# Kernel optimization log

Measured on AMD Instinct MI355X. Metric: run time of the kernel, lower is better.

The kernel has to match this reference:

```python
import jax, jax.numpy as jnp
import numpy as np
from math import sqrt


def _build_transitions(dim):
    # Upper-triangular (i<=j) pairs in the same row-major order as the torch loop.
    iu0, iu1 = np.triu_indices(dim)
    n_mono = len(iu0)
    idx = np.arange(n_mono)
    M = np.zeros((dim, dim), dtype=np.int32)
    M[iu0, iu1] = idx
    M[iu1, iu0] = idx
    coef_trans = np.full((n_mono, 1), sqrt(2.0), dtype=np.float32)
    coef_trans[idx[iu0 == iu1]] = 1.0  # diagonal coefficients stay scale 1
    return iu0, iu1, M.reshape(-1), coef_trans


def setup_inputs() -> dict:
    key = jax.random.key(0)
    k1, k2, k3, k4 = jax.random.split(key, 4)
    dim, n_quadrics, B = 512, 64, 2048
    n_mono = dim * (dim - 1) // 2 + dim  # 131328
    points = jax.random.normal(k1, (B, dim), dtype=jnp.float32)
    # orthogonal-ish init is only an init detail; random normal keeps math identical
    q_coefs = jax.random.normal(k2, (n_mono, n_quadrics), dtype=jnp.float32) / np.sqrt(n_mono)
    l_coefs = 2.0 * jax.random.uniform(k3, (dim, n_quadrics), dtype=jnp.float32) - 1.0
    free_coefs = 2.0 * jax.random.uniform(k4, (1, n_quadrics), dtype=jnp.float32) - 1.0
    return {"points": points, "q_coefs": q_coefs, "l_coefs": l_coefs, "free_coefs": free_coefs}


def reference(points, q_coefs, l_coefs, free_coefs):
    B, dim = points.shape
    nq = q_coefs.shape[1]
    iu0, iu1, inds_trans, coef_trans_np = _build_transitions(dim)
    coef_trans = jnp.asarray(coef_trans_np)

    # quadratic monomials: q[b, k] = p[b, i_k] * p[b, j_k]  (upper-tri order)
    q = points[:, iu0] * points[:, iu1]  # (B, n_mono)

    coefs = q_coefs * coef_trans  # (n_mono, nq) real coefficients

    # values of quadrics at points
    values = jnp.abs(q @ coefs + points @ l_coefs + free_coefs)  # (B, nq)

    # symmetric full matrices gathered from flat coefficient vector
    m_full = coefs[inds_trans].reshape(dim, dim, nq)  # (dim, dim, nq)
    dm = (jnp.eye(dim, dtype=points.dtype) + 1.0)[:, :, None]  # 2 on diag, ... wait: eye+ones -> 2 diag, 1 off
    m_scaled = m_full * dm

    # gradients: grad[b, k, e] = sum_d p[b, d] * m_scaled[d, e, k] + l_coefs[e, k]
    q_grad = jnp.einsum("bd,dek->bke", points, m_scaled) + l_coefs.T[None, :, :]  # (B, nq, dim)
    grad = jnp.sum(q_grad * q_grad, axis=2)  # (B, nq)

    norm = jnp.linalg.norm(q_coefs, axis=0)  # (nq,)
    scores = (jnp.sqrt(grad / 4.0 + values * norm) - jnp.sqrt(grad) / 2.0) / norm
    return scores
```

## Files before the change

kernel.cpp:

```cpp
#include <hip/hip_runtime.h>

#define DIM 512
#define NQ 64
#define BATCH 2048

typedef __bf16  bf16x8  __attribute__((ext_vector_type(8)));
typedef float   floatx4 __attribute__((ext_vector_type(4)));

static __device__ inline unsigned short f2bf(float f) {
    unsigned int u = __float_as_uint(f);
    return (unsigned short)((u + 0x7fffu + ((u >> 16) & 1u)) >> 16);
}
static __device__ inline float bf2f(unsigned short h) {
    return __uint_as_float((unsigned int)h << 16);
}
static __device__ inline unsigned int pack2(float a, float b) {
    return (unsigned)f2bf(a) | ((unsigned)f2bf(b) << 16);
}

__global__ __launch_bounds__(512, 3)
void hsq_expand_kernel(const float* __restrict__ qc,
                       const float* __restrict__ pts,
                       unsigned short* __restrict__ W,
                       unsigned short* __restrict__ Pb,
                       float* __restrict__ npart) {
    const int e = blockIdx.x;

    if (blockIdx.y == 4) {
        const int i4 = e * 512 + threadIdx.x;
        const float4 v = *(const float4*)(pts + (size_t)i4 * 4);
        uint2 wv;
        wv.x = pack2(v.x, v.y); wv.y = pack2(v.z, v.w);
        *(uint2*)(Pb + (size_t)i4 * 4) = wv;
        return;
    }

    const int dblk = blockIdx.y;
    const int pb   = dblk * 512 + e;
    const int wid  = threadIdx.x >> 6;
    const int k    = threadIdx.x & 63;
    const int d0   = dblk * 128 + wid * 16;

    __shared__ unsigned short tv[64 * 136];
    __shared__ float part[8][64];

    float v[16];
#pragma unroll
    for (int s = 0; s < 16; ++s) {
        const int d = d0 + s;
        const int i = d < e ? d : e;
        const int j = d < e ? e : d;
        const int idx = i * DIM - ((i * (i - 1)) >> 1) + (j - i);
        v[s] = qc[(size_t)idx * NQ + k];
    }

    float nacc = 0.0f;
#pragma unroll
    for (int s = 0; s < 16; ++s)
        if (d0 + s >= e) nacc += v[s] * v[s];

#pragma unroll
    for (int t = 0; t < 2; ++t) {
        float sc[8];
#pragma unroll
        for (int q = 0; q < 8; ++q) {
            const int d = d0 + t * 8 + q;
            sc[q] = v[t * 8 + q] * ((d == e) ? 2.0f : 1.41421356237309515f);
        }
        uint4 w;
        w.x = pack2(sc[0], sc[1]); w.y = pack2(sc[2], sc[3]);
        w.z = pack2(sc[4], sc[5]); w.w = pack2(sc[6], sc[7]);
        *(uint4*)&tv[k * 136 + wid * 16 + t * 8] = w;
    }
    part[wid][k] = nacc;
    __syncthreads();

#pragma unroll
    for (int r = 0; r < 2; ++r) {
        const int kk = r * 32 + (threadIdx.x >> 4);
        const int u  = threadIdx.x & 15;
        const uint4 w = *(const uint4*)&tv[kk * 136 + u * 8];
        *(uint4*)(W + ((size_t)(kk * DIM + e)) * DIM + dblk * 128 + u * 8) = w;
    }
    if (threadIdx.x < 64) {
        npart[(size_t)k * 2048 + pb] =
            part[0][k] + part[1][k] + part[2][k] + part[3][k] +
            part[4][k] + part[5][k] + part[6][k] + part[7][k];
    }
}

__global__ __launch_bounds__(512, 2)
void hsq_gemm_kernel(const unsigned short* __restrict__ Pb,
                     const unsigned short* __restrict__ W,
                     const float* __restrict__ l_coefs,
                     float2* __restrict__ part) {
    extern __shared__ unsigned short smem[];

    const int bid = blockIdx.x;
    const int wg  = (bid & 7) * 128 + (bid >> 3);
    const int k   = wg >> 4;
    const int rem = wg & 15;
    const int et  = rem >> 3;
    const int mt  = rem & 7;
    const int m0  = mt * 256;

    const int tid  = threadIdx.x;
    const int lane = tid & 63;
    const int w    = tid >> 6;
    const int wm   = w >> 2;
    const int wn   = w & 3;
    const int c    = lane & 15;
    const int quad = lane >> 4;

    const unsigned short* Wk = W + ((size_t)k * DIM + (size_t)et * 256) * DIM;

    const int scolb = ((tid & 7) * 16) ^ (((tid >> 3) & 7) << 4);
    const unsigned short* pAs = Pb + (size_t)(m0 + (tid >> 3)) * DIM + (scolb >> 1);
    const unsigned short* pBs = Wk + (size_t)(tid >> 3) * DIM + (scolb >> 1);

    const int xorv  = (c & 7) << 4;
    const int koff0 = ((0 * 64 + quad * 16) ^ xorv) >> 1;
    const int koff1 = ((1 * 64 + quad * 16) ^ xorv) >> 1;
    const int awoff = wm * 8192 + c * 64;
    const int bwoff = (wn >> 1) * 8192 + (wn & 1) * 4096 + c * 64;

#define STAGE_HALF(LDSELEM, GSRC) do {                                         \
    _Pragma("unroll")                                                          \
    for (int cc_ = 0; cc_ < 2; ++cc_) {                                        \
        __builtin_amdgcn_global_load_lds(                                      \
            (const __attribute__((address_space(1))) unsigned int*)            \
                ((GSRC) + (size_t)(cc_ * 64) * DIM),                           \
            (__attribute__((address_space(3))) unsigned int*)                  \
                (smem + (LDSELEM) + cc_ * 4096 + tid * 8),                     \
            16, 0, 0);                                                         \
    }                                                                          \
} while (0)

#define LOADB(BBASE) do {                                                      \
    _Pragma("unroll")                                                          \
    for (int ni_ = 0; ni_ < 4; ++ni_) {                                        \
        bfr[ni_][0] = *(const bf16x8*)(smem + (BBASE) + bwoff + ni_ * 1024 + koff0); \
        bfr[ni_][1] = *(const bf16x8*)(smem + (BBASE) + bwoff + ni_ * 1024 + koff1); \
    }                                                                          \
} while (0)

#define PHASE(ABASE, MI0, PRE_B, STAGE_AND_WAIT) do {                          \
    bf16x8 a00 = *(const bf16x8*)(smem + (ABASE) + awoff + (MI0) * 1024 + koff0);     \
    bf16x8 a01 = *(const bf16x8*)(smem + (ABASE) + awoff + (MI0) * 1024 + koff1);     \
    bf16x8 a10 = *(const bf16x8*)(smem + (ABASE) + awoff + ((MI0) + 1) * 1024 + koff0); \
    bf16x8 a11 = *(const bf16x8*)(smem + (ABASE) + awoff + ((MI0) + 1) * 1024 + koff1); \
    PRE_B;                                                                     \
    STAGE_AND_WAIT;                                                            \
    asm volatile("" ::: "memory");                                             \
    __builtin_amdgcn_s_barrier();                                              \
    asm volatile("" ::: "memory");                                             \
    __builtin_amdgcn_s_setprio(1);                                             \
    _Pragma("unroll")                                                          \
    for (int ni_ = 0; ni_ < 4; ++ni_) {                                        \
        acc[(MI0)][ni_]     = __builtin_amdgcn_mfma_f32_16x16x32_bf16(a00, bfr[ni_][0], acc[(MI0)][ni_], 0, 0, 0);     \
        acc[(MI0)][ni_]     = __builtin_amdgcn_mfma_f32_16x16x32_bf16(a01, bfr[ni_][1], acc[(MI0)][ni_], 0, 0, 0);     \
        acc[(MI0) + 1][ni_] = __builtin_amdgcn_mfma_f32_16x16x32_bf16(a10, bfr[ni_][0], acc[(MI0) + 1][ni_], 0, 0, 0); \
        acc[(MI0) + 1][ni_] = __builtin_amdgcn_mfma_f32_16x16x32_bf16(a11, bfr[ni_][1], acc[(MI0) + 1][ni_], 0, 0, 0); \
    }                                                                          \
    __builtin_amdgcn_s_setprio(0);                                             \
    asm volatile("" ::: "memory");                                             \
    __builtin_amdgcn_s_barrier();                                              \
    asm volatile("" ::: "memory");                                             \
} while (0)

    floatx4 acc[8][4];
#pragma unroll
    for (int mi = 0; mi < 8; ++mi)
#pragma unroll
        for (int ni = 0; ni < 4; ++ni)
            acc[mi][ni] = (floatx4){0.f, 0.f, 0.f, 0.f};

    bf16x8 bfr[4][2];

    STAGE_HALF(0,             pAs);
    STAGE_HALF(8192,          pAs + 128 * DIM);
    STAGE_HALF(16384,         pBs);
    STAGE_HALF(16384 + 8192,  pBs + 128 * DIM);
    STAGE_HALF(49152,         pBs + 64);
    STAGE_HALF(49152 + 8192,  pBs + 128 * DIM + 64);
    asm volatile("s_waitcnt vmcnt(4)" ::: "memory");
    __builtin_amdgcn_s_barrier();
    asm volatile("" ::: "memory");

    for (int it = 0; it < 4; ++it) {
        const unsigned short* pA1 = pAs + (size_t)(2 * it + 1) * 64;
        const unsigned short* pB2 = pBs + (size_t)(2 * it + 2) * 64;
        const unsigned short* pA2 = pAs + (size_t)(2 * it + 2) * 64;
        const unsigned short* pB3 = pBs + (size_t)(2 * it + 3) * 64;

        PHASE(0, 0, LOADB(16384), { STAGE_HALF(32768, pA1); });
        PHASE(0, 2, ((void)0),    { STAGE_HALF(32768 + 8192, pA1 + 128 * DIM); });
        PHASE(0, 4, ((void)0),    { if (it < 3) STAGE_HALF(16384, pB2); });
        PHASE(0, 6, ((void)0), {
            if (it < 3) {
                STAGE_HALF(16384 + 8192, pB2 + 128 * DIM);
                asm volatile("s_waitcnt vmcnt(4)" ::: "memory");
            } else {
                asm volatile("s_waitcnt vmcnt(0)" ::: "memory");
            }
        });
        PHASE(32768, 0, LOADB(49152), { if (it < 3) STAGE_HALF(0, pA2); });
        PHASE(32768, 2, ((void)0),    { if (it < 3) STAGE_HALF(8192, pA2 + 128 * DIM); });
        PHASE(32768, 4, ((void)0),    { if (it < 3) STAGE_HALF(49152, pB3); });
        PHASE(32768, 6, ((void)0), {
            if (it < 3) {
                STAGE_HALF(49152 + 8192, pB3 + 128 * DIM);
                asm volatile("s_waitcnt vmcnt(4)" ::: "memory");
            }
        });
    }
#undef PHASE
#undef LOADB
#undef STAGE_HALF

    __syncthreads();

    float lcv[4];
#pragma unroll
    for (int ni = 0; ni < 4; ++ni)
        lcv[ni] = l_coefs[(et * 256 + wn * 64 + ni * 16 + c) * NQ + k];

    const unsigned short* Pe = Pb + (size_t)(m0 + wm * 128) * DIM + et * 256 + wn * 64 + c;
    float* red = (float*)smem;

#pragma unroll
    for (int mi = 0; mi < 8; ++mi)
#pragma unroll
        for (int r = 0; r < 4; ++r) {
            const unsigned short* Prow = Pe + (size_t)(mi * 16 + quad * 4 + r) * DIM;
            float pv = 0.f, pg = 0.f;
#pragma unroll
            for (int ni = 0; ni < 4; ++ni) {
                const float g = acc[mi][ni][r];
                const float l = lcv[ni];
                pv += bf2f(Prow[ni * 16]) * (0.5f * g + l);
                const float gq = g + l;
                pg += gq * gq;
            }
#pragma unroll
            for (int off = 1; off < 16; off <<= 1) {
                pv += __shfl_xor(pv, off);
                pg += __shfl_xor(pg, off);
            }
            if (c == 0) {
                const int row16 = mi * 16 + quad * 4 + r;
                red[(w * 128 + row16) * 2 + 0] = pv;
                red[(w * 128 + row16) * 2 + 1] = pg;
            }
        }
    __syncthreads();

    if (tid < 256) {
        const int row16 = tid & 127;
        const int wmf   = tid >> 7;
        float pv = 0.f, pg = 0.f;
#pragma unroll
        for (int wnf = 0; wnf < 4; ++wnf) {
            const int wi = wmf * 4 + wnf;
            pv += red[(wi * 128 + row16) * 2 + 0];
            pg += red[(wi * 128 + row16) * 2 + 1];
        }
        part[((size_t)(et * NQ + k)) * BATCH + m0 + wmf * 128 + row16] =
            make_float2(pv, pg);
    }
}

__global__ void hsq_final_kernel(const float2* __restrict__ part,
                                 const float* __restrict__ npart,
                                 const float* __restrict__ free_coefs,
                                 float* __restrict__ out) {
    const int k = blockIdx.x;
    const int t = threadIdx.x;
    __shared__ float ws[4];

    const float4* src = (const float4*)(npart + (size_t)k * 2048);
    const float4 a = src[t * 2], b = src[t * 2 + 1];
    float s = a.x + a.y + a.z + a.w + b.x + b.y + b.z + b.w;
#pragma unroll
    for (int off = 1; off < 64; off <<= 1) s += __shfl_xor(s, off);
    if ((t & 63) == 0) ws[t >> 6] = s;
    __syncthreads();
    const float nrm = sqrtf(ws[0] + ws[1] + ws[2] + ws[3]);
    const float fc  = free_coefs[k];

#pragma unroll
    for (int i = 0; i < 8; ++i) {
        const int bidx = i * 256 + t;
        float pv = 0.f, pg = 0.f;
#pragma unroll
        for (int eb = 0; eb < 2; ++eb) {
            const float2 p = part[((size_t)(eb * NQ + k)) * BATCH + bidx];
            pv += p.x; pg += p.y;
        }
        const float vals = fabsf(pv + fc);
        out[(size_t)bidx * NQ + k] = (sqrtf(0.25f * pg + vals * nrm) - 0.5f * sqrtf(pg)) / nrm;
    }
}

extern "C" void kernel_launch(void* const* d_in, const int* in_sizes, int n_in,
                              void* d_out, int out_size, void* d_ws, size_t ws_size,
                              hipStream_t stream) {
    const float* points     = (const float*)d_in[0];
    const float* q_coefs    = (const float*)d_in[1];
    const float* l_coefs    = (const float*)d_in[2];
    const float* free_coefs = (const float*)d_in[3];
    float* out = (float*)d_out;

    char* ws = (char*)d_ws;
    unsigned short* W  = (unsigned short*)ws;
    unsigned short* Pb = (unsigned short*)(ws + 33554432);
    float2*         part  = (float2*)(ws + 35651584);
    float*          npart = (float*)(ws + 37748736);

    static bool attr_done = false;
    if (!attr_done) {
        (void)hipFuncSetAttribute((const void*)hsq_gemm_kernel,
                                  hipFuncAttributeMaxDynamicSharedMemorySize,
                                  131072);
        attr_done = true;
    }

    hsq_expand_kernel<<<dim3(512, 5), 512, 0, stream>>>(q_coefs, points, W, Pb, npart);
    hsq_gemm_kernel<<<dim3(1024), dim3(512), 131072, stream>>>(Pb, W, l_coefs, part);
    hsq_final_kernel<<<dim3(NQ), 256, 0, stream>>>(part, npart, free_coefs, out);
}
```

Before: 191.6 us.

## Shrink GEMM tile to 256x128 with triple-buffered K=32 pipeline

The gradient GEMM now splits each quadric's output dimension into four 128-wide tiles instead of two 256-wide tiles. This doubles the grid to 2048 blocks and halves the per-wave accumulator set to 4x4 MFMA tiles. K is staged in 32-element chunks through a three-slot LDS ring using direct global-to-LDS loads, with a new swizzle. LDS per block drops from 128 KB to about 76 KB, and launch bounds are raised to target more resident waves. In exchange, the tiles are less arithmetically intense, more barriers are issued per K, and the partial-sum buffer and final reduction grow to four e-blocks.

```diff
diff --git a/kernel.cpp b/kernel.cpp
--- a/kernel.cpp
+++ b/kernel.cpp
@@ -89,7 +89,7 @@
     }
 }
 
-__global__ __launch_bounds__(512, 2)
+__global__ __launch_bounds__(512, 4)
 void hsq_gemm_kernel(const unsigned short* __restrict__ Pb,
                      const unsigned short* __restrict__ W,
                      const float* __restrict__ l_coefs,
@@ -97,9 +97,9 @@
     extern __shared__ unsigned short smem[];
 
     const int bid = blockIdx.x;
-    const int wg  = (bid & 7) * 128 + (bid >> 3);
-    const int k   = wg >> 4;
-    const int rem = wg & 15;
+    const int wg  = (bid & 7) * 256 + (bid >> 3);
+    const int k   = wg >> 5;
+    const int rem = wg & 31;
     const int et  = rem >> 3;
     const int mt  = rem & 7;
     const int m0  = mt * 256;
@@ -107,129 +107,128 @@
     const int tid  = threadIdx.x;
     const int lane = tid & 63;
     const int w    = tid >> 6;
-    const int wm   = w >> 2;
-    const int wn   = w & 3;
+    const int wm   = w >> 1;
+    const int wn   = w & 1;
     const int c    = lane & 15;
     const int quad = lane >> 4;
 
-    const unsigned short* Wk = W + ((size_t)k * DIM + (size_t)et * 256) * DIM;
-
-    const int scolb = ((tid & 7) * 16) ^ (((tid >> 3) & 7) << 4);
-    const unsigned short* pAs = Pb + (size_t)(m0 + (tid >> 3)) * DIM + (scolb >> 1);
-    const unsigned short* pBs = Wk + (size_t)(tid >> 3) * DIM + (scolb >> 1);
-
-    const int xorv  = (c & 7) << 4;
-    const int koff0 = ((0 * 64 + quad * 16) ^ xorv) >> 1;
-    const int koff1 = ((1 * 64 + quad * 16) ^ xorv) >> 1;
-    const int awoff = wm * 8192 + c * 64;
-    const int bwoff = (wn >> 1) * 8192 + (wn & 1) * 4096 + c * 64;
-
-#define STAGE_HALF(LDSELEM, GSRC) do {                                         \
+    const unsigned short* aptr0;
+    const unsigned short* aptr1;
+    const unsigned short* bptr;
+    {
+        int slot = tid;
+        int p = slot >> 3;
+        int x = ((slot & 7) ^ (p & 7)) << 4;
+        aptr0 = Pb + (size_t)(m0 + (p << 1) + (x >> 6)) * DIM + ((x & 63) >> 1);
+        slot = 512 + tid;
+        p = slot >> 3;
+        x = ((slot & 7) ^ (p & 7)) << 4;
+        aptr1 = Pb + (size_t)(m0 + (p << 1) + (x >> 6)) * DIM + ((x & 63) >> 1);
+        slot = tid;
+        p = slot >> 3;
+        x = ((slot & 7) ^ (p & 7)) << 4;
+        bptr = W + (size_t)k * DIM * DIM
+                 + (size_t)(et * 128 + (p << 1) + (x >> 6)) * DIM + ((x & 63) >> 1);
+    }
+
+    int aoff[4], boff[4];
+#pragma unroll
+    for (int mi = 0; mi < 4; ++mi) {
+        const int row  = wm * 64 + mi * 16 + c;
+        const int line = row >> 1;
+        const int inb  = (((row & 1) << 6) | (quad << 4)) ^ ((line & 7) << 4);
+        aoff[mi] = line * 64 + (inb >> 1);
+    }
+#pragma unroll
+    for (int ni = 0; ni < 4; ++ni) {
+        const int row  = wn * 64 + ni * 16 + c;
+        const int line = row >> 1;
+        const int inb  = (((row & 1) << 6) | (quad << 4)) ^ ((line & 7) << 4);
+        boff[ni] = line * 64 + (inb >> 1);
+    }
+
+#define STAGE3(SB, T) do {                                                     \
+    __builtin_amdgcn_global_load_lds(                                          \
+        (const __attribute__((address_space(1))) unsigned int*)(aptr0 + (T) * 32), \
+        (__attribute__((address_space(3))) unsigned int*)(smem + (SB) * 12288 + tid * 8), \
+        16, 0, 0);                                                             \
+    __builtin_amdgcn_global_load_lds(                                          \
+        (const __attribute__((address_space(1))) unsigned int*)(aptr1 + (T) * 32), \
+        (__attribute__((address_space(3))) unsigned int*)(smem + (SB) * 12288 + 4096 + tid * 8), \
+        16, 0, 0);                                                             \
+    __builtin_amdgcn_global_load_lds(                                          \
+        (const __attribute__((address_space(1))) unsigned int*)(bptr + (T) * 32), \
+        (__attribute__((address_space(3))) unsigned int*)(smem + (SB) * 12288 + 8192 + tid * 8), \
+        16, 0, 0);                                                             \
+} while (0)
+
+#define KITER(TB, STAGE_STMT, WAIT_STMT) do {                                  \
+    STAGE_STMT;                                                                \
+    bf16x8 afr[4], bfr[4];                                                     \
     _Pragma("unroll")                                                          \
-    for (int cc_ = 0; cc_ < 2; ++cc_) {                                        \
-        __builtin_amdgcn_global_load_lds(                                      \
-            (const __attribute__((address_space(1))) unsigned int*)            \
-                ((GSRC) + (size_t)(cc_ * 64) * DIM),                           \
-            (__attribute__((address_space(3))) unsigned int*)                  \
-                (smem + (LDSELEM) + cc_ * 4096 + tid * 8),                     \
-            16, 0, 0);                                                         \
-    }                                                                          \
-} while (0)
-
-#define LOADB(BBASE) do {                                                      \
+    for (int mi = 0; mi < 4; ++mi)                                             \
+        afr[mi] = *(const bf16x8*)(smem + (TB) * 12288 + aoff[mi]);            \
     _Pragma("unroll")                                                          \
-    for (int ni_ = 0; ni_ < 4; ++ni_) {                                        \
-        bfr[ni_][0] = *(const bf16x8*)(smem + (BBASE) + bwoff + ni_ * 1024 + koff0); \
-        bfr[ni_][1] = *(const bf16x8*)(smem + (BBASE) + bwoff + ni_ * 1024 + koff1); \
-    }                                                                          \
-} while (0)
-
-#define PHASE(ABASE, MI0, PRE_B, STAGE_AND_WAIT) do {                          \
-    bf16x8 a00 = *(const bf16x8*)(smem + (ABASE) + awoff + (MI0) * 1024 + koff0);     \
-    bf16x8 a01 = *(const bf16x8*)(smem + (ABASE) + awoff + (MI0) * 1024 + koff1);     \
-    bf16x8 a10 = *(const bf16x8*)(smem + (ABASE) + awoff + ((MI0) + 1) * 1024 + koff0); \
-    bf16x8 a11 = *(const bf16x8*)(smem + (ABASE) + awoff + ((MI0) + 1) * 1024 + koff1); \
-    PRE_B;                                                                     \
-    STAGE_AND_WAIT;                                                            \
-    asm volatile("" ::: "memory");                                             \
-    __builtin_amdgcn_s_barrier();                                              \
-    asm volatile("" ::: "memory");                                             \
+    for (int ni = 0; ni < 4; ++ni)                                             \
+        bfr[ni] = *(const bf16x8*)(smem + (TB) * 12288 + 8192 + boff[ni]);     \
     __builtin_amdgcn_s_setprio(1);                                             \
     _Pragma("unroll")                                                          \
-    for (int ni_ = 0; ni_ < 4; ++ni_) {                                        \
-        acc[(MI0)][ni_]     = __builtin_amdgcn_mfma_f32_16x16x32_bf16(a00, bfr[ni_][0], acc[(MI0)][ni_], 0, 0, 0);     \
-        acc[(MI0)][ni_]     = __builtin_amdgcn_mfma_f32_16x16x32_bf16(a01, bfr[ni_][1], acc[(MI0)][ni_], 0, 0, 0);     \
-        acc[(MI0) + 1][ni_] = __builtin_amdgcn_mfma_f32_16x16x32_bf16(a10, bfr[ni_][0], acc[(MI0) + 1][ni_], 0, 0, 0); \
-        acc[(MI0) + 1][ni_] = __builtin_amdgcn_mfma_f32_16x16x32_bf16(a11, bfr[ni_][1], acc[(MI0) + 1][ni_], 0, 0, 0); \
-    }                                                                          \
+    for (int mi = 0; mi < 4; ++mi)                                             \
+        _Pragma("unroll")                                                      \
+        for (int ni = 0; ni < 4; ++ni)                                         \
+            acc[mi][ni] = __builtin_amdgcn_mfma_f32_16x16x32_bf16(             \
+                afr[mi], bfr[ni], acc[mi][ni], 0, 0, 0);                       \
     __builtin_amdgcn_s_setprio(0);                                             \
+    WAIT_STMT;                                                                 \
     asm volatile("" ::: "memory");                                             \
     __builtin_amdgcn_s_barrier();                                              \
     asm volatile("" ::: "memory");                                             \
 } while (0)
 
-    floatx4 acc[8][4];
-#pragma unroll
-    for (int mi = 0; mi < 8; ++mi)
+#define VM3  asm volatile("s_waitcnt vmcnt(3)" ::: "memory")
+#define VM0  asm volatile("s_waitcnt vmcnt(0)" ::: "memory")
+
+    floatx4 acc[4][4];
+#pragma unroll
+    for (int mi = 0; mi < 4; ++mi)
 #pragma unroll
         for (int ni = 0; ni < 4; ++ni)
             acc[mi][ni] = (floatx4){0.f, 0.f, 0.f, 0.f};
 
-    bf16x8 bfr[4][2];
-
-    STAGE_HALF(0,             pAs);
-    STAGE_HALF(8192,          pAs + 128 * DIM);
-    STAGE_HALF(16384,         pBs);
-    STAGE_HALF(16384 + 8192,  pBs + 128 * DIM);
-    STAGE_HALF(49152,         pBs + 64);
-    STAGE_HALF(49152 + 8192,  pBs + 128 * DIM + 64);
-    asm volatile("s_waitcnt vmcnt(4)" ::: "memory");
+    STAGE3(0, 0);
+    STAGE3(1, 1);
+    VM3;
     __builtin_amdgcn_s_barrier();
     asm volatile("" ::: "memory");
 
-    for (int it = 0; it < 4; ++it) {
-        const unsigned short* pA1 = pAs + (size_t)(2 * it + 1) * 64;
-        const unsigned short* pB2 = pBs + (size_t)(2 * it + 2) * 64;
-        const unsigned short* pA2 = pAs + (size_t)(2 * it + 2) * 64;
-        const unsigned short* pB3 = pBs + (size_t)(2 * it + 3) * 64;
-
-        PHASE(0, 0, LOADB(16384), { STAGE_HALF(32768, pA1); });
-        PHASE(0, 2, ((void)0),    { STAGE_HALF(32768 + 8192, pA1 + 128 * DIM); });
-        PHASE(0, 4, ((void)0),    { if (it < 3) STAGE_HALF(16384, pB2); });
-        PHASE(0, 6, ((void)0), {
-            if (it < 3) {
-                STAGE_HALF(16384 + 8192, pB2 + 128 * DIM);
-                asm volatile("s_waitcnt vmcnt(4)" ::: "memory");
-            } else {
-                asm volatile("s_waitcnt vmcnt(0)" ::: "memory");
-            }
-        });
-        PHASE(32768, 0, LOADB(49152), { if (it < 3) STAGE_HALF(0, pA2); });
-        PHASE(32768, 2, ((void)0),    { if (it < 3) STAGE_HALF(8192, pA2 + 128 * DIM); });
-        PHASE(32768, 4, ((void)0),    { if (it < 3) STAGE_HALF(49152, pB3); });
-        PHASE(32768, 6, ((void)0), {
-            if (it < 3) {
-                STAGE_HALF(49152 + 8192, pB3 + 128 * DIM);
-                asm volatile("s_waitcnt vmcnt(4)" ::: "memory");
-            }
-        });
-    }
-#undef PHASE
-#undef LOADB
-#undef STAGE_HALF
+#pragma unroll 1
+    for (int tt = 0; tt < 12; tt += 3) {
+        KITER(0, STAGE3(2, tt + 2), VM3);
+        KITER(1, STAGE3(0, tt + 3), VM3);
+        KITER(2, STAGE3(1, tt + 4), VM3);
+    }
+    KITER(0, STAGE3(2, 14), VM3);
+    KITER(1, STAGE3(0, 15), VM3);
+    KITER(2, ((void)0), VM0);
+    KITER(0, ((void)0), ((void)0));
+
+#undef KITER
+#undef STAGE3
+#undef VM3
+#undef VM0
 
     __syncthreads();
 
     float lcv[4];
 #pragma unroll
     for (int ni = 0; ni < 4; ++ni)
-        lcv[ni] = l_coefs[(et * 256 + wn * 64 + ni * 16 + c) * NQ + k];
-
-    const unsigned short* Pe = Pb + (size_t)(m0 + wm * 128) * DIM + et * 256 + wn * 64 + c;
-    float* red = (float*)smem;
-
-#pragma unroll
-    for (int mi = 0; mi < 8; ++mi)
+        lcv[ni] = l_coefs[(et * 128 + wn * 64 + ni * 16 + c) * NQ + k];
+
+    const unsigned short* Pe = Pb + (size_t)(m0 + wm * 64) * DIM + et * 128 + wn * 64 + c;
+    float* red = (float*)&smem[36864];
+
+#pragma unroll
+    for (int mi = 0; mi < 4; ++mi)
 #pragma unroll
         for (int r = 0; r < 4; ++r) {
             const unsigned short* Prow = Pe + (size_t)(mi * 16 + quad * 4 + r) * DIM;
@@ -248,25 +247,17 @@
                 pg += __shfl_xor(pg, off);
             }
             if (c == 0) {
-                const int row16 = mi * 16 + quad * 4 + r;
-                red[(w * 128 + row16) * 2 + 0] = pv;
-                red[(w * 128 + row16) * 2 + 1] = pg;
+                const int row = wm * 64 + mi * 16 + quad * 4 + r;
+                red[(wn * 256 + row) * 2 + 0] = pv;
+                red[(wn * 256 + row) * 2 + 1] = pg;
             }
         }
     __syncthreads();
 
     if (tid < 256) {
-        const int row16 = tid & 127;
-        const int wmf   = tid >> 7;
-        float pv = 0.f, pg = 0.f;
-#pragma unroll
-        for (int wnf = 0; wnf < 4; ++wnf) {
-            const int wi = wmf * 4 + wnf;
-            pv += red[(wi * 128 + row16) * 2 + 0];
-            pg += red[(wi * 128 + row16) * 2 + 1];
-        }
-        part[((size_t)(et * NQ + k)) * BATCH + m0 + wmf * 128 + row16] =
-            make_float2(pv, pg);
+        const float pv = red[tid * 2 + 0] + red[(256 + tid) * 2 + 0];
+        const float pg = red[tid * 2 + 1] + red[(256 + tid) * 2 + 1];
+        part[((size_t)(et * NQ + k)) * BATCH + m0 + tid] = make_float2(pv, pg);
     }
 }
 
@@ -293,7 +284,7 @@
         const int bidx = i * 256 + t;
         float pv = 0.f, pg = 0.f;
 #pragma unroll
-        for (int eb = 0; eb < 2; ++eb) {
+        for (int eb = 0; eb < 4; ++eb) {
             const float2 p = part[((size_t)(eb * NQ + k)) * BATCH + bidx];
             pv += p.x; pg += p.y;
         }
@@ -315,17 +306,17 @@
     unsigned short* W  = (unsigned short*)ws;
     unsigned short* Pb = (unsigned short*)(ws + 33554432);
     float2*         part  = (float2*)(ws + 35651584);
-    float*          npart = (float*)(ws + 37748736);
+    float*          npart = (float*)(ws + 39845888);
 
     static bool attr_done = false;
     if (!attr_done) {
         (void)hipFuncSetAttribute((const void*)hsq_gemm_kernel,
                                   hipFuncAttributeMaxDynamicSharedMemorySize,
-                                  131072);
+                                  77824);
         attr_done = true;
     }
 
     hsq_expand_kernel<<<dim3(512, 5), 512, 0, stream>>>(q_coefs, points, W, Pb, npart);
-    hsq_gemm_kernel<<<dim3(1024), dim3(512), 131072, stream>>>(Pb, W, l_coefs, part);
+    hsq_gemm_kernel<<<dim3(2048), dim3(512), 77824, stream>>>(Pb, W, l_coefs, part);
     hsq_final_kernel<<<dim3(NQ), 256, 0, stream>>>(part, npart, free_coefs, out);
 }
```

New measurement: 193.1 us. No clear change (+0.8%).
